# Kernel tuning notes

Measured on AMD Instinct MI355X. Metric: run time of the kernel, lower is better.

## Reference

```python
import jax, jax.numpy as jnp
import numpy as np

B, L, D = 4096, 200, 128
EPS = 1e-12  # Keras l2_normalize epsilon


def _l2_normalize(x):
    # K.l2_normalize: x / sqrt(max(sum(x^2), eps))
    sq = jnp.sum(x * x, axis=-1, keepdims=True)
    return x * jax.lax.rsqrt(jnp.maximum(sq, EPS))


def setup_inputs() -> dict:
    key = jax.random.key(0)
    k1, k2, k3, k4 = jax.random.split(key, 4)
    return {
        "recentTimeRepresentations": jax.random.normal(k1, (B, L, D), dtype=jnp.float32),
        "curTimeRepresentation": jax.random.normal(k2, (B, D), dtype=jnp.float32),
        "recentTimestamps": jax.random.randint(k3, (B, L), 0, 2, dtype=jnp.int32),
        "recentItemEmbeddings": jax.random.normal(k4, (B, L, D), dtype=jnp.float32),
    }


def reference(recentTimeRepresentations, curTimeRepresentation, recentTimestamps, recentItemEmbeddings):
    mask = (recentTimestamps > 0).astype(jnp.float32)  # [B, L]
    cur_n = _l2_normalize(curTimeRepresentation)        # [B, D]
    rec_n = _l2_normalize(recentTimeRepresentations)    # [B, L, D]
    # cosine similarity of current rep vs each history rep
    similarity = jnp.einsum("bd,bld->bl", cur_n, rec_n)  # [B, L]
    masked_similarity = mask * ((similarity + 1.0) * 0.5)  # [B, L]
    # weighted sum of history item embeddings (no softmax)
    userHistoryRepresentation = jnp.einsum("bl,bld->bd", masked_similarity, recentItemEmbeddings)
    return userHistoryRepresentation
```

## Files before the change

kernel.cpp:

```cpp
#include <hip/hip_runtime.h>

#define B_ 4096
#define L_ 200
#define D_ 128

__global__ __launch_bounds__(256, 8) void tahe_kernel(
    const float* __restrict__ rec,
    const float* __restrict__ cur,
    const int*   __restrict__ ts,
    const float* __restrict__ item,
    float*       __restrict__ out)
{
    const int b   = blockIdx.x;
    const int tid = threadIdx.x;

    __shared__ int    s_act[L_];
    __shared__ float  s_w[L_];
    __shared__ int    s_n;
    __shared__ float  s_cinv;
    __shared__ float4 s_red[8][32];

    if (tid == 0) s_n = 0;
    __syncthreads();

    if (tid < L_) {
        if (ts[b * L_ + tid] > 0) {
            int p = atomicAdd(&s_n, 1);
            s_act[p] = tid;
        }
    }

    if (tid < 32) {
        const float4 c4 = *(const float4*)(cur + b * D_ + tid * 4);
        float ss = c4.x*c4.x + c4.y*c4.y + c4.z*c4.z + c4.w*c4.w;
        #pragma unroll
        for (int m = 1; m <= 16; m <<= 1) ss += __shfl_xor(ss, m);
        if (tid == 0) {
            float r = rsqrtf(fmaxf(ss, 1e-12f));
            r = r * (1.5f - 0.5f * ss * r * r);
            s_cinv = r;
        }
    }
    __syncthreads();

    const int   n    = s_n;
    const float cinv = s_cinv;
    const float* recb  = rec  + (size_t)b * (L_ * D_);
    const float* itemb = item + (size_t)b * (L_ * D_);

    {
        const int g8 = tid >> 3;
        const int j  = tid & 7;
        float4 c[4];
        #pragma unroll
        for (int k = 0; k < 4; ++k)
            c[k] = *(const float4*)(cur + b * D_ + (j + 8 * k) * 4);

        for (int i = g8; i < n; i += 32) {
            const int l = s_act[i];
            const float* r = recb + (size_t)l * D_;
            float pd = 0.f, ps = 0.f;
            #pragma unroll
            for (int k = 0; k < 4; ++k) {
                const float4 r4 = *(const float4*)(r + (j + 8 * k) * 4);
                pd = fmaf(c[k].x, r4.x, fmaf(c[k].y, r4.y, fmaf(c[k].z, r4.z, fmaf(c[k].w, r4.w, pd))));
                ps = fmaf(r4.x, r4.x, fmaf(r4.y, r4.y, fmaf(r4.z, r4.z, fmaf(r4.w, r4.w, ps))));
            }
            #pragma unroll
            for (int m = 1; m <= 4; m <<= 1) {
                pd += __shfl_xor(pd, m);
                ps += __shfl_xor(ps, m);
            }
            if (j == 0) {
                float rs = rsqrtf(fmaxf(ps, 1e-12f));
                rs = rs * (1.5f - 0.5f * ps * rs * rs);
                s_w[i] = fmaf(pd * rs * cinv, 0.5f, 0.5f);
            }
        }
    }
    __syncthreads();

    const int g   = tid >> 5;
    const int sub = tid & 31;
    float4 acc = make_float4(0.f, 0.f, 0.f, 0.f);

    for (int i = g; i < n; i += 8) {
        const int   l = s_act[i];
        const float w = s_w[i];
        const float4 t4 = *(const float4*)(itemb + (size_t)l * D_ + sub * 4);
        acc.x = fmaf(w, t4.x, acc.x);
        acc.y = fmaf(w, t4.y, acc.y);
        acc.z = fmaf(w, t4.z, acc.z);
        acc.w = fmaf(w, t4.w, acc.w);
    }

    s_red[g][sub] = acc;
    __syncthreads();

    if (tid < D_) {
        const int chunk = tid >> 2, comp = tid & 3;
        float v = 0.f;
        #pragma unroll
        for (int gg = 0; gg < 8; ++gg) {
            const float* rf = (const float*)&s_red[gg][chunk];
            v += rf[comp];
        }
        out[b * D_ + tid] = v;
    }
}

extern "C" void kernel_launch(void* const* d_in, const int* in_sizes, int n_in,
                              void* d_out, int out_size, void* d_ws, size_t ws_size,
                              hipStream_t stream) {
    const float* rec  = (const float*)d_in[0];
    const float* cur  = (const float*)d_in[1];
    const int*   ts   = (const int*)d_in[2];
    const float* item = (const float*)d_in[3];
    float*       out  = (float*)d_out;
    tahe_kernel<<<B_, 256, 0, stream>>>(rec, cur, ts, item, out);
}
```

Baseline: 702.8 us.

## Fuse similarity and weighted-sum phases into a single per-row loop

Merges the two phases (cosine weight computation, then weighted item accumulation) into one loop. Each 32-lane group now computes the dot product and norm for a row with a full 32-lane shuffle reduction and immediately accumulates the item row, which removes the shared weight array and one block barrier. The loop is unrolled by two so four row loads are issued together for more memory-level parallelism. The cost is more shuffle work per row, since every group reduces across 32 lanes instead of 8.

```diff
diff --git a/kernel.cpp b/kernel.cpp
--- a/kernel.cpp
+++ b/kernel.cpp
@@ -15,9 +15,7 @@
     const int tid = threadIdx.x;
 
     __shared__ int    s_act[L_];
-    __shared__ float  s_w[L_];
     __shared__ int    s_n;
-    __shared__ float  s_cinv;
     __shared__ float4 s_red[8][32];
 
     if (tid == 0) s_n = 0;
@@ -30,71 +28,79 @@
         }
     }
 
-    if (tid < 32) {
-        const float4 c4 = *(const float4*)(cur + b * D_ + tid * 4);
-        float ss = c4.x*c4.x + c4.y*c4.y + c4.z*c4.z + c4.w*c4.w;
-        #pragma unroll
-        for (int m = 1; m <= 16; m <<= 1) ss += __shfl_xor(ss, m);
-        if (tid == 0) {
-            float r = rsqrtf(fmaxf(ss, 1e-12f));
-            r = r * (1.5f - 0.5f * ss * r * r);
-            s_cinv = r;
-        }
-    }
+    const int hw  = tid >> 5;
+    const int sub = tid & 31;
+
+    const float4 c4 = *(const float4*)(cur + (size_t)b * D_ + sub * 4);
+    float css = fmaf(c4.x, c4.x, fmaf(c4.y, c4.y, fmaf(c4.z, c4.z, c4.w * c4.w)));
+    #pragma unroll
+    for (int m = 1; m <= 16; m <<= 1) css += __shfl_xor(css, m);
+    float cinv = rsqrtf(fmaxf(css, 1e-12f));
+    cinv = cinv * (1.5f - 0.5f * css * cinv * cinv);
+
     __syncthreads();
+    const int n = s_n;
 
-    const int   n    = s_n;
-    const float cinv = s_cinv;
     const float* recb  = rec  + (size_t)b * (L_ * D_);
     const float* itemb = item + (size_t)b * (L_ * D_);
 
-    {
-        const int g8 = tid >> 3;
-        const int j  = tid & 7;
-        float4 c[4];
-        #pragma unroll
-        for (int k = 0; k < 4; ++k)
-            c[k] = *(const float4*)(cur + b * D_ + (j + 8 * k) * 4);
-
-        for (int i = g8; i < n; i += 32) {
-            const int l = s_act[i];
-            const float* r = recb + (size_t)l * D_;
-            float pd = 0.f, ps = 0.f;
-            #pragma unroll
-            for (int k = 0; k < 4; ++k) {
-                const float4 r4 = *(const float4*)(r + (j + 8 * k) * 4);
-                pd = fmaf(c[k].x, r4.x, fmaf(c[k].y, r4.y, fmaf(c[k].z, r4.z, fmaf(c[k].w, r4.w, pd))));
-                ps = fmaf(r4.x, r4.x, fmaf(r4.y, r4.y, fmaf(r4.z, r4.z, fmaf(r4.w, r4.w, ps))));
-            }
-            #pragma unroll
-            for (int m = 1; m <= 4; m <<= 1) {
-                pd += __shfl_xor(pd, m);
-                ps += __shfl_xor(ps, m);
-            }
-            if (j == 0) {
-                float rs = rsqrtf(fmaxf(ps, 1e-12f));
-                rs = rs * (1.5f - 0.5f * ps * rs * rs);
-                s_w[i] = fmaf(pd * rs * cinv, 0.5f, 0.5f);
-            }
-        }
-    }
-    __syncthreads();
-
-    const int g   = tid >> 5;
-    const int sub = tid & 31;
     float4 acc = make_float4(0.f, 0.f, 0.f, 0.f);
 
-    for (int i = g; i < n; i += 8) {
-        const int   l = s_act[i];
-        const float w = s_w[i];
-        const float4 t4 = *(const float4*)(itemb + (size_t)l * D_ + sub * 4);
-        acc.x = fmaf(w, t4.x, acc.x);
-        acc.y = fmaf(w, t4.y, acc.y);
-        acc.z = fmaf(w, t4.z, acc.z);
-        acc.w = fmaf(w, t4.w, acc.w);
+    int i = hw;
+    for (; i + 8 < n; i += 16) {
+        const int l0 = s_act[i];
+        const int l1 = s_act[i + 8];
+        const float4 r0 = *(const float4*)(recb  + (size_t)l0 * D_ + sub * 4);
+        const float4 t0 = *(const float4*)(itemb + (size_t)l0 * D_ + sub * 4);
+        const float4 r1 = *(const float4*)(recb  + (size_t)l1 * D_ + sub * 4);
+        const float4 t1 = *(const float4*)(itemb + (size_t)l1 * D_ + sub * 4);
+
+        float pd0 = fmaf(c4.x, r0.x, fmaf(c4.y, r0.y, fmaf(c4.z, r0.z, c4.w * r0.w)));
+        float ps0 = fmaf(r0.x, r0.x, fmaf(r0.y, r0.y, fmaf(r0.z, r0.z, r0.w * r0.w)));
+        float pd1 = fmaf(c4.x, r1.x, fmaf(c4.y, r1.y, fmaf(c4.z, r1.z, c4.w * r1.w)));
+        float ps1 = fmaf(r1.x, r1.x, fmaf(r1.y, r1.y, fmaf(r1.z, r1.z, r1.w * r1.w)));
+
+        #pragma unroll
+        for (int m = 1; m <= 16; m <<= 1) {
+            pd0 += __shfl_xor(pd0, m);
+            ps0 += __shfl_xor(ps0, m);
+            pd1 += __shfl_xor(pd1, m);
+            ps1 += __shfl_xor(ps1, m);
+        }
+
+        float rs0 = rsqrtf(fmaxf(ps0, 1e-12f));
+        rs0 = rs0 * (1.5f - 0.5f * ps0 * rs0 * rs0);
+        float rs1 = rsqrtf(fmaxf(ps1, 1e-12f));
+        rs1 = rs1 * (1.5f - 0.5f * ps1 * rs1 * rs1);
+        const float w0 = fmaf(pd0 * rs0 * cinv, 0.5f, 0.5f);
+        const float w1 = fmaf(pd1 * rs1 * cinv, 0.5f, 0.5f);
+
+        acc.x = fmaf(w1, t1.x, fmaf(w0, t0.x, acc.x));
+        acc.y = fmaf(w1, t1.y, fmaf(w0, t0.y, acc.y));
+        acc.z = fmaf(w1, t1.z, fmaf(w0, t0.z, acc.z));
+        acc.w = fmaf(w1, t1.w, fmaf(w0, t0.w, acc.w));
+    }
+    if (i < n) {
+        const int l0 = s_act[i];
+        const float4 r0 = *(const float4*)(recb  + (size_t)l0 * D_ + sub * 4);
+        const float4 t0 = *(const float4*)(itemb + (size_t)l0 * D_ + sub * 4);
+        float pd0 = fmaf(c4.x, r0.x, fmaf(c4.y, r0.y, fmaf(c4.z, r0.z, c4.w * r0.w)));
+        float ps0 = fmaf(r0.x, r0.x, fmaf(r0.y, r0.y, fmaf(r0.z, r0.z, r0.w * r0.w)));
+        #pragma unroll
+        for (int m = 1; m <= 16; m <<= 1) {
+            pd0 += __shfl_xor(pd0, m);
+            ps0 += __shfl_xor(ps0, m);
+        }
+        float rs0 = rsqrtf(fmaxf(ps0, 1e-12f));
+        rs0 = rs0 * (1.5f - 0.5f * ps0 * rs0 * rs0);
+        const float w0 = fmaf(pd0 * rs0 * cinv, 0.5f, 0.5f);
+        acc.x = fmaf(w0, t0.x, acc.x);
+        acc.y = fmaf(w0, t0.y, acc.y);
+        acc.z = fmaf(w0, t0.z, acc.z);
+        acc.w = fmaf(w0, t0.w, acc.w);
     }
 
-    s_red[g][sub] = acc;
+    s_red[hw][sub] = acc;
     __syncthreads();
 
     if (tid < D_) {
@@ -105,7 +111,7 @@
             const float* rf = (const float*)&s_red[gg][chunk];
             v += rf[comp];
         }
-        out[b * D_ + tid] = v;
+        out[(size_t)b * D_ + tid] = v;
     }
 }
 
```

Result: no change. 702.8 us (+0.0%).
